# Performance work log

Measured on AMD Instinct MI355X. Metric: run time of the kernel, lower is better.

## Reference

```python
import jax, jax.numpy as jnp
import numpy as np

OPS_SIZE = (40, 40, 40)
ALPHA = 0.005
BETA = 0.01


def _disp_from_landmarks(coords, values):
    # coords, values: (N,3). Returns (3, W0, H0, D0) coarse displacement field.
    D0, H0, W0 = OPS_SIZE
    axes = [jnp.linspace(-1.0, 1.0, s) for s in OPS_SIZE]
    grid = jnp.stack(jnp.meshgrid(*axes, indexing='ij'), -1).reshape(-1, 3)  # (G,3)
    # squared distance ||g - c||^2 via expansion (avoids (N,G,3) repeat tensor)
    d2 = (jnp.sum(grid * grid, -1)[:, None]
          + jnp.sum(coords * coords, -1)[None, :]
          - 2.0 * grid @ coords.T)  # (G,N)
    w = jnp.exp(-d2 / ALPHA)
    w = (BETA + 1.0) * w / (jnp.sum(w, axis=1, keepdims=True) + BETA)
    disp = (w @ values).reshape(D0, H0, W0, 3)
    return jnp.transpose(disp, (3, 2, 1, 0))  # torch permute(3,2,1,0)


def _interp_axis(x, axis, out_s):
    # 1D linear resize along `axis`, matching F.interpolate align_corners=False
    in_s = x.shape[axis]
    c = jnp.maximum((jnp.arange(out_s, dtype=jnp.float32) + 0.5) * (in_s / out_s) - 0.5, 0.0)
    i0 = jnp.minimum(jnp.floor(c).astype(jnp.int32), in_s - 1)
    i1 = jnp.minimum(i0 + 1, in_s - 1)
    t = (c - i0.astype(jnp.float32)).astype(x.dtype)
    shp = [1] * x.ndim
    shp[axis] = out_s
    t = t.reshape(shp)
    return jnp.take(x, i0, axis=axis) * (1 - t) + jnp.take(x, i1, axis=axis) * t


def _resize_trilinear(x, out_size):
    # x: (C, d, h, w) -> (C, D, H, W); trilinear resize is separable
    for ax, s in zip((1, 2, 3), out_size):
        x = _interp_axis(x, ax, s)
    return x


def _grid_sample_3d(vol, grid):
    # vol: (B,C,D,H,W), grid: (B,Do,Ho,Wo,3), grid[...,0]=x indexes W.
    # mode='bilinear' (trilinear), padding_mode='zeros', align_corners=False
    B, C, D, H, W = vol.shape
    x = ((grid[..., 0] + 1.0) * W - 1.0) / 2.0
    y = ((grid[..., 1] + 1.0) * H - 1.0) / 2.0
    z = ((grid[..., 2] + 1.0) * D - 1.0) / 2.0

    def per_batch(v, x, y, z):
        x0 = jnp.floor(x); y0 = jnp.floor(y); z0 = jnp.floor(z)
        fx = x - x0; fy = y - y0; fz = z - z0
        x0i = x0.astype(jnp.int32); y0i = y0.astype(jnp.int32); z0i = z0.astype(jnp.int32)
        acc = jnp.zeros((C,) + x.shape, v.dtype)
        for dz in (0, 1):
            wz = fz if dz else 1.0 - fz
            zi = z0i + dz
            for dy in (0, 1):
                wy = fy if dy else 1.0 - fy
                yi = y0i + dy
                for dx in (0, 1):
                    wx = fx if dx else 1.0 - fx
                    xi = x0i + dx
                    m = ((zi >= 0) & (zi < D) & (yi >= 0) & (yi < H) & (xi >= 0) & (xi < W)).astype(v.dtype)
                    zc = jnp.clip(zi, 0, D - 1); yc = jnp.clip(yi, 0, H - 1); xc = jnp.clip(xi, 0, W - 1)
                    acc = acc + v[:, zc, yc, xc] * ((wz * wy * wx * m)[None])
        return acc

    return jax.vmap(per_batch)(vol, x, y, z)


def reference(orgin_mask, control_points_coords, control_points_offsets):
    B, C, D, H, W = orgin_mask.shape
    coords = control_points_coords + control_points_offsets  # (B,N,3)
    vals = -control_points_offsets                            # (B,N,3)
    disp = jax.vmap(_disp_from_landmarks)(coords, vals)       # (B,3,W0,H0,D0)
    flow = jax.vmap(lambda d: _resize_trilinear(d, (D, H, W)))(disp)  # (B,3,D,H,W)
    axes = [jnp.linspace(-1.0, 1.0, s) for s in (D, H, W)]
    base = jnp.stack(jnp.meshgrid(*axes, indexing='ij'), 0)   # (3,D,H,W)
    base = jnp.transpose(base, (0, 3, 2, 1))                  # torch permute(0,1,4,3,2); needs D==H==W
    warped = base[None] + flow                                # (B,3,D,H,W)
    warped = jnp.transpose(warped, (0, 2, 3, 4, 1))           # (B,D,H,W,3)
    return _grid_sample_3d(orgin_mask, warped)


def setup_inputs() -> dict:
    key = jax.random.key(0)
    k1, k2, k3 = jax.random.split(key, 3)
    orgin_mask = jax.random.uniform(k1, (2, 1, 128, 128, 128), dtype=jnp.float32)
    control_points_coords = jax.random.uniform(k2, (2, 1024, 3), dtype=jnp.float32, minval=-1.0, maxval=1.0)
    control_points_offsets = jax.random.normal(k3, (2, 1024, 3), dtype=jnp.float32) * 0.05
    return {"orgin_mask": orgin_mask,
            "control_points_coords": control_points_coords,
            "control_points_offsets": control_points_offsets}
```

## Files before the change

kernel.cpp:

```cpp
#include <hip/hip_runtime.h>
#include <math.h>
#include <string.h>

#define NLM   1024
#define NB    2
#define OPS   40
#define DIM   128
#define OPS3  (OPS*OPS*OPS)
#define DIM3  (DIM*DIM*DIM)

#define P_T 4
#define Q_T 4
#define R_T 8
#define NP  (OPS/P_T)
#define NQ  (OPS/Q_T)
#define NR  (OPS/R_T)
#define MARGIN 0.30f

#define K2f  (-288.5390081777927f)
#define M2f  ( 577.0780163555854f)


__device__ __forceinline__ float fexp2(float x) {
#if __has_builtin(__builtin_amdgcn_exp2f)
    return __builtin_amdgcn_exp2f(x);
#else
    return exp2f(x);
#endif
}

__global__ __launch_bounds__(128)
void coarse_kernel(const float* __restrict__ coords, const float* __restrict__ offs,
                   float4* __restrict__ C) {
    __shared__ float4 sA[NLM];
    __shared__ float4 sV[NLM];
    __shared__ int sCnt;

    const int t = threadIdx.x;
    const int b = blockIdx.y;
    const int tile = blockIdx.x;
    const int tp = tile / (NQ*NR);
    const int tq = (tile / NR) % NQ;
    const int tr = tile % NR;

    const float step = 2.f / (OPS - 1);
    const float bx0 = -1.f + step * (tr*R_T)          - MARGIN;
    const float bx1 = -1.f + step * (tr*R_T + R_T-1)  + MARGIN;
    const float by0 = -1.f + step * (tq*Q_T)          - MARGIN;
    const float by1 = -1.f + step * (tq*Q_T + Q_T-1)  + MARGIN;
    const float bz0 = -1.f + step * (tp*P_T)          - MARGIN;
    const float bz1 = -1.f + step * (tp*P_T + P_T-1)  + MARGIN;

    if (t == 0) sCnt = 0;
    __syncthreads();

    for (int n = t; n < NLM; n += 128) {
        const float* cp = coords + (b*NLM + n)*3;
        const float* op = offs   + (b*NLM + n)*3;
        float ox = op[0], oy = op[1], oz = op[2];
        float cx = cp[0] + ox, cy = cp[1] + oy, cz = cp[2] + oz;
        if (cx >= bx0 && cx <= bx1 && cy >= by0 && cy <= by1 &&
            cz >= bz0 && cz <= bz1) {
            int idx = atomicAdd(&sCnt, 1);
            sA[idx] = make_float4(cx, cy, cz, K2f*(cx*cx + cy*cy + cz*cz));
            sV[idx] = make_float4(-ox, -oy, -oz, 0.f);
        }
    }
    __syncthreads();
    const int cnt = sCnt;

    const int lp = t >> 5;
    const int lq = (t >> 3) & 3;
    const int lr = t & 7;
    const float gx = -1.f + step * (tr*R_T + lr);
    const float gy = -1.f + step * (tq*Q_T + lq);
    const float gz = -1.f + step * (tp*P_T + lp);
    const float h  = K2f * (gx*gx + gy*gy + gz*gz);

    float aS = 0.f, aX = 0.f, aY = 0.f, aZ = 0.f;
    for (int n = 0; n < cnt; ++n) {
        float4 a = sA[n];
        float4 v = sV[n];
        float u   = fmaf(gx, a.x, fmaf(gy, a.y, gz*a.z));
        float arg = fmaf(M2f, u, h + a.w);
        float e   = fexp2(arg);
        aS += e;
        aX = fmaf(e, v.x, aX);
        aY = fmaf(e, v.y, aY);
        aZ = fmaf(e, v.z, aZ);
    }

    const int p = tp*P_T + lp, q = tq*Q_T + lq, r = tr*R_T + lr;
    const float inv = 1.01f / (aS + 0.01f);
    C[b*OPS3 + (p*OPS + q)*OPS + r] = make_float4(aX*inv, aY*inv, aZ*inv, 0.f);
}

__device__ __forceinline__ void axis_interp(int t, int& a0, int& a1, float& w) {
    float c = fmaxf(0.3125f * (float)t - 0.34375f, 0.f);
    float f = floorf(c);
    a0 = (int)f;
    a1 = min(a0 + 1, OPS - 1);
    w = c - f;
}

__device__ __forceinline__ float4 lerp4(float4 a, float4 b, float t) {
    return make_float4(a.x + t*(b.x - a.x),
                       a.y + t*(b.y - a.y),
                       a.z + t*(b.z - a.z),
                       0.f);
}

typedef float vf2 __attribute__((ext_vector_type(2)));

#if __has_builtin(__builtin_amdgcn_make_buffer_rsrc) && \
    __has_builtin(__builtin_amdgcn_raw_ptr_buffer_load_b64)
#define USE_BUF 1
typedef unsigned int v2u __attribute__((ext_vector_type(2)));
__device__ __forceinline__ vf2 bload2(__amdgpu_buffer_rsrc_t R, int voff_bytes) {
    v2u r = __builtin_amdgcn_raw_ptr_buffer_load_b64(R, voff_bytes, 0, 0);
    vf2 f;
    memcpy(&f, &r, 8);
    return f;
}
#else
#define USE_BUF 0
struct __attribute__((packed, aligned(4))) P2 { vf2 v; };
__device__ __forceinline__ vf2 load2(const float* p) {
    return ((const P2*)p)->v;
}
#endif

struct AW {
    int r0, r1, r2, r3, xs;
    float e0, e1, wy0, wy1, wz0, wz1;
};

__device__ __forceinline__ AW make_aw(float px, float py, float pz) {
    AW s;
    float xf = floorf(px), yf = floorf(py), zf = floorf(pz);
    int x0 = (int)xf, y0 = (int)yf, z0 = (int)zf;
    float ax = px - xf, ay = py - yf, az = pz - zf;

    float wx0 = ((unsigned)x0     < 128u) ? (1.f - ax) : 0.f;
    float wx1 = ((unsigned)(x0+1) < 128u) ? ax         : 0.f;
    s.wy0 = ((unsigned)y0     < 128u) ? (1.f - ay) : 0.f;
    s.wy1 = ((unsigned)(y0+1) < 128u) ? ay         : 0.f;
    s.wz0 = ((unsigned)z0     < 128u) ? (1.f - az) : 0.f;
    s.wz1 = ((unsigned)(z0+1) < 128u) ? az         : 0.f;

    s.xs = min(max(x0, 0), 126);
    int d = x0 - s.xs;
    s.e0 = (d == 0) ? wx0 : ((d == -1) ? wx1 : 0.f);
    s.e1 = (d == 0) ? wx1 : ((d ==  1) ? wx0 : 0.f);

#if USE_BUF
    int ya = y0 << 7, yb2 = (y0+1) << 7;
    int za = z0 << 14, zb2 = (z0+1) << 14;
#else
    int ya = (y0 & 127) << 7, yb2 = ((y0+1) & 127) << 7;
    int za = (z0 & 127) << 14, zb2 = ((z0+1) & 127) << 14;
#endif
    s.r0 = za + ya;  s.r1 = za + yb2;
    s.r2 = zb2 + ya; s.r3 = zb2 + yb2;
    return s;
}

__global__ __launch_bounds__(512)
void warp_kernel(const float* __restrict__ mask, const float4* __restrict__ C,
                 float* __restrict__ out) {
    __shared__ float4 sF[8][OPS];

    const int g = blockIdx.x;
    const int w = threadIdx.x >> 6;
    const int lane = threadIdx.x & 63;
    const int line = ((g & 7) << 12) + ((g >> 3) << 3) + w;
    const int j = line & (DIM-1);
    const int i = (line >> 7) & (DIM-1);
    const int b = line >> 14;

    int i0,i1,j0,j1; float ti,tj;
    axis_interp(i, i0, i1, ti);
    axis_interp(j, j0, j1, tj);

    const float4* Cb = C + b*OPS3;
    if (lane < OPS) {
        float4 c00 = Cb[(i0*OPS + j0)*OPS + lane];
        float4 c01 = Cb[(i0*OPS + j1)*OPS + lane];
        float4 c10 = Cb[(i1*OPS + j0)*OPS + lane];
        float4 c11 = Cb[(i1*OPS + j1)*OPS + lane];
        sF[w][lane] = lerp4(lerp4(c00, c01, tj), lerp4(c10, c11, tj), ti);
    }

    const float* M = mask + b * DIM3;
#if USE_BUF
    __amdgpu_buffer_rsrc_t R =
        __builtin_amdgcn_make_buffer_rsrc((void*)M, (short)0,
                                          DIM3 * 4, 0x00020000);
#endif
    const float s127 = 2.f / (DIM - 1);
    const float yb = -1.f + s127 * (float)j;
    const float zb = -1.f + s127 * (float)i;

    AW aw[2];
    #pragma unroll
    for (int c = 0; c < 2; ++c) {
        const int k = lane + (c << 6);
        int k0,k1; float tk;
        axis_interp(k, k0, k1, tk);
        float4 fl = lerp4(sF[w][k0], sF[w][k1], tk);
        float x = -1.f + s127 * (float)k + fl.x;
        float y = yb + fl.y;
        float z = zb + fl.z;
        aw[c] = make_aw(((x + 1.f) * (float)DIM - 1.f) * 0.5f,
                        ((y + 1.f) * (float)DIM - 1.f) * 0.5f,
                        ((z + 1.f) * (float)DIM - 1.f) * 0.5f);
    }

    vf2 t0[4], t1[4];
#if USE_BUF
    {
        const AW& s = aw[0];
        t0[0] = bload2(R, (s.r0 + s.xs) * 4);
        t0[1] = bload2(R, (s.r1 + s.xs) * 4);
        t0[2] = bload2(R, (s.r2 + s.xs) * 4);
        t0[3] = bload2(R, (s.r3 + s.xs) * 4);
    }
    {
        const AW& s = aw[1];
        t1[0] = bload2(R, (s.r0 + s.xs) * 4);
        t1[1] = bload2(R, (s.r1 + s.xs) * 4);
        t1[2] = bload2(R, (s.r2 + s.xs) * 4);
        t1[3] = bload2(R, (s.r3 + s.xs) * 4);
    }
#else
    {
        const AW& s = aw[0];
        t0[0] = load2(M + s.r0 + s.xs);
        t0[1] = load2(M + s.r1 + s.xs);
        t0[2] = load2(M + s.r2 + s.xs);
        t0[3] = load2(M + s.r3 + s.xs);
    }
    {
        const AW& s = aw[1];
        t1[0] = load2(M + s.r0 + s.xs);
        t1[1] = load2(M + s.r1 + s.xs);
        t1[2] = load2(M + s.r2 + s.xs);
        t1[3] = load2(M + s.r3 + s.xs);
    }
#endif

    float res[2];
    #pragma unroll
    for (int c = 0; c < 2; ++c) {
        const AW& s = aw[c];
        const vf2* tv = c ? t1 : t0;
        vf2 e;  e.x = s.e0;  e.y = s.e1;
        vf2 acc;
        acc    = tv[0] * (e * (s.wz0*s.wy0));
        acc   += tv[1] * (e * (s.wz0*s.wy1));
        acc   += tv[2] * (e * (s.wz1*s.wy0));
        acc   += tv[3] * (e * (s.wz1*s.wy1));
        res[c] = acc.x + acc.y;
    }
    out[(line << 7) + lane]      = res[0];
    out[(line << 7) + lane + 64] = res[1];
}

extern "C" void kernel_launch(void* const* d_in, const int* in_sizes, int n_in,
                              void* d_out, int out_size, void* d_ws, size_t ws_size,
                              hipStream_t stream) {
    const float* mask   = (const float*)d_in[0];
    const float* coords = (const float*)d_in[1];
    const float* offs   = (const float*)d_in[2];
    float* out = (float*)d_out;

    float4* coarse = (float4*)d_ws;

    dim3 g1(NP*NQ*NR, NB);
    coarse_kernel<<<g1, 128, 0, stream>>>(coords, offs, coarse);

    warp_kernel<<<NB*DIM*DIM/8, 512, 0, stream>>>(mask, coarse, out);
}
```

Before: 98.35 us.

## Assign adjacent x pairs per thread and share one 16-byte gather

Each thread now handles two adjacent output voxels along x instead of two voxels 64 apart. When both samples fall in the same y/z cell and adjacent x columns, four 128-bit loads replace eight 64-bit loads, and the outputs are written as one float2 store. Otherwise it falls back to the old eight-load path. Block size also drops from 512 to 256 threads with a matching grid, which adds a divergent branch and changes the occupancy mix.

```diff
diff --git a/kernel.cpp b/kernel.cpp
--- a/kernel.cpp
+++ b/kernel.cpp
@@ -111,27 +111,33 @@
 }
 
 typedef float vf2 __attribute__((ext_vector_type(2)));
+typedef float vf4 __attribute__((ext_vector_type(4)));
 
 #if __has_builtin(__builtin_amdgcn_make_buffer_rsrc) && \
-    __has_builtin(__builtin_amdgcn_raw_ptr_buffer_load_b64)
+    __has_builtin(__builtin_amdgcn_raw_ptr_buffer_load_b64) && \
+    __has_builtin(__builtin_amdgcn_raw_ptr_buffer_load_b128)
 #define USE_BUF 1
 typedef unsigned int v2u __attribute__((ext_vector_type(2)));
+typedef unsigned int v4u __attribute__((ext_vector_type(4)));
 __device__ __forceinline__ vf2 bload2(__amdgpu_buffer_rsrc_t R, int voff_bytes) {
     v2u r = __builtin_amdgcn_raw_ptr_buffer_load_b64(R, voff_bytes, 0, 0);
-    vf2 f;
-    memcpy(&f, &r, 8);
-    return f;
+    vf2 f; memcpy(&f, &r, 8); return f;
+}
+__device__ __forceinline__ vf4 bload4(__amdgpu_buffer_rsrc_t R, int voff_bytes) {
+    v4u r = __builtin_amdgcn_raw_ptr_buffer_load_b128(R, voff_bytes, 0, 0);
+    vf4 f; memcpy(&f, &r, 16); return f;
 }
 #else
 #define USE_BUF 0
 struct __attribute__((packed, aligned(4))) P2 { vf2 v; };
-__device__ __forceinline__ vf2 load2(const float* p) {
-    return ((const P2*)p)->v;
-}
+struct __attribute__((packed, aligned(4))) P4 { vf4 v; };
+__device__ __forceinline__ vf2 load2(const float* p) { return ((const P2*)p)->v; }
+__device__ __forceinline__ vf4 load4(const float* p) { return ((const P4*)p)->v; }
 #endif
 
 struct AW {
     int r0, r1, r2, r3, xs;
+    int y0, z0;
     float e0, e1, wy0, wy1, wz0, wz1;
 };
 
@@ -153,6 +159,7 @@
     s.e0 = (d == 0) ? wx0 : ((d == -1) ? wx1 : 0.f);
     s.e1 = (d == 0) ? wx1 : ((d ==  1) ? wx0 : 0.f);
 
+    s.y0 = y0; s.z0 = z0;
 #if USE_BUF
     int ya = y0 << 7, yb2 = (y0+1) << 7;
     int za = z0 << 14, zb2 = (z0+1) << 14;
@@ -165,15 +172,15 @@
     return s;
 }
 
-__global__ __launch_bounds__(512)
+__global__ __launch_bounds__(256)
 void warp_kernel(const float* __restrict__ mask, const float4* __restrict__ C,
                  float* __restrict__ out) {
-    __shared__ float4 sF[8][OPS];
+    __shared__ float4 sF[4][OPS];
 
     const int g = blockIdx.x;
     const int w = threadIdx.x >> 6;
     const int lane = threadIdx.x & 63;
-    const int line = ((g & 7) << 12) + ((g >> 3) << 3) + w;
+    const int line = ((g & 7) << 12) + ((g >> 3) << 2) + w;
     const int j = line & (DIM-1);
     const int i = (line >> 7) & (DIM-1);
     const int b = line >> 14;
@@ -204,7 +211,7 @@
     AW aw[2];
     #pragma unroll
     for (int c = 0; c < 2; ++c) {
-        const int k = lane + (c << 6);
+        const int k = (lane << 1) + c;
         int k0,k1; float tk;
         axis_interp(k, k0, k1, tk);
         float4 fl = lerp4(sF[w][k0], sF[w][k1], tk);
@@ -216,54 +223,92 @@
                         ((z + 1.f) * (float)DIM - 1.f) * 0.5f);
     }
 
-    vf2 t0[4], t1[4];
+    const AW& A = aw[0];
+    const AW& B = aw[1];
+    const bool fast = (A.y0 == B.y0) & (A.z0 == B.z0) &
+                      (B.xs - A.xs == 1) & (A.xs <= 124);
+
+    float resA, resB;
+    if (fast) {
+        vf4 T0, T1, T2, T3;
 #if USE_BUF
-    {
-        const AW& s = aw[0];
-        t0[0] = bload2(R, (s.r0 + s.xs) * 4);
-        t0[1] = bload2(R, (s.r1 + s.xs) * 4);
-        t0[2] = bload2(R, (s.r2 + s.xs) * 4);
-        t0[3] = bload2(R, (s.r3 + s.xs) * 4);
-    }
-    {
-        const AW& s = aw[1];
-        t1[0] = bload2(R, (s.r0 + s.xs) * 4);
-        t1[1] = bload2(R, (s.r1 + s.xs) * 4);
-        t1[2] = bload2(R, (s.r2 + s.xs) * 4);
-        t1[3] = bload2(R, (s.r3 + s.xs) * 4);
-    }
-#else
-    {
-        const AW& s = aw[0];
-        t0[0] = load2(M + s.r0 + s.xs);
-        t0[1] = load2(M + s.r1 + s.xs);
-        t0[2] = load2(M + s.r2 + s.xs);
-        t0[3] = load2(M + s.r3 + s.xs);
-    }
-    {
-        const AW& s = aw[1];
-        t1[0] = load2(M + s.r0 + s.xs);
-        t1[1] = load2(M + s.r1 + s.xs);
-        t1[2] = load2(M + s.r2 + s.xs);
-        t1[3] = load2(M + s.r3 + s.xs);
-    }
-#endif
-
-    float res[2];
-    #pragma unroll
-    for (int c = 0; c < 2; ++c) {
-        const AW& s = aw[c];
-        const vf2* tv = c ? t1 : t0;
-        vf2 e;  e.x = s.e0;  e.y = s.e1;
-        vf2 acc;
-        acc    = tv[0] * (e * (s.wz0*s.wy0));
-        acc   += tv[1] * (e * (s.wz0*s.wy1));
-        acc   += tv[2] * (e * (s.wz1*s.wy0));
-        acc   += tv[3] * (e * (s.wz1*s.wy1));
-        res[c] = acc.x + acc.y;
-    }
-    out[(line << 7) + lane]      = res[0];
-    out[(line << 7) + lane + 64] = res[1];
+        T0 = bload4(R, (A.r0 + A.xs) * 4);
+        T1 = bload4(R, (A.r1 + A.xs) * 4);
+        T2 = bload4(R, (A.r2 + A.xs) * 4);
+        T3 = bload4(R, (A.r3 + A.xs) * 4);
+#else
+        T0 = load4(M + A.r0 + A.xs);
+        T1 = load4(M + A.r1 + A.xs);
+        T2 = load4(M + A.r2 + A.xs);
+        T3 = load4(M + A.r3 + A.xs);
+#endif
+        float a0 = A.wz0*A.wy0, a1 = A.wz0*A.wy1;
+        float a2 = A.wz1*A.wy0, a3 = A.wz1*A.wy1;
+        float b0 = B.wz0*B.wy0, b1 = B.wz0*B.wy1;
+        float b2 = B.wz1*B.wy0, b3 = B.wz1*B.wy1;
+        float rA;
+        rA = T0.x * (a0*A.e0);
+        rA = fmaf(T0.y, a0*A.e1, rA);
+        rA = fmaf(T1.x, a1*A.e0, rA);
+        rA = fmaf(T1.y, a1*A.e1, rA);
+        rA = fmaf(T2.x, a2*A.e0, rA);
+        rA = fmaf(T2.y, a2*A.e1, rA);
+        rA = fmaf(T3.x, a3*A.e0, rA);
+        rA = fmaf(T3.y, a3*A.e1, rA);
+        float rB;
+        rB = T0.y * (b0*B.e0);
+        rB = fmaf(T0.z, b0*B.e1, rB);
+        rB = fmaf(T1.y, b1*B.e0, rB);
+        rB = fmaf(T1.z, b1*B.e1, rB);
+        rB = fmaf(T2.y, b2*B.e0, rB);
+        rB = fmaf(T2.z, b2*B.e1, rB);
+        rB = fmaf(T3.y, b3*B.e0, rB);
+        rB = fmaf(T3.z, b3*B.e1, rB);
+        resA = rA; resB = rB;
+    } else {
+        vf2 t0[4], t1[4];
+#if USE_BUF
+        t0[0] = bload2(R, (A.r0 + A.xs) * 4);
+        t0[1] = bload2(R, (A.r1 + A.xs) * 4);
+        t0[2] = bload2(R, (A.r2 + A.xs) * 4);
+        t0[3] = bload2(R, (A.r3 + A.xs) * 4);
+        t1[0] = bload2(R, (B.r0 + B.xs) * 4);
+        t1[1] = bload2(R, (B.r1 + B.xs) * 4);
+        t1[2] = bload2(R, (B.r2 + B.xs) * 4);
+        t1[3] = bload2(R, (B.r3 + B.xs) * 4);
+#else
+        t0[0] = load2(M + A.r0 + A.xs);
+        t0[1] = load2(M + A.r1 + A.xs);
+        t0[2] = load2(M + A.r2 + A.xs);
+        t0[3] = load2(M + A.r3 + A.xs);
+        t1[0] = load2(M + B.r0 + B.xs);
+        t1[1] = load2(M + B.r1 + B.xs);
+        t1[2] = load2(M + B.r2 + B.xs);
+        t1[3] = load2(M + B.r3 + B.xs);
+#endif
+        float rA;
+        rA = t0[0].x * (A.wz0*A.wy0*A.e0);
+        rA = fmaf(t0[0].y, A.wz0*A.wy0*A.e1, rA);
+        rA = fmaf(t0[1].x, A.wz0*A.wy1*A.e0, rA);
+        rA = fmaf(t0[1].y, A.wz0*A.wy1*A.e1, rA);
+        rA = fmaf(t0[2].x, A.wz1*A.wy0*A.e0, rA);
+        rA = fmaf(t0[2].y, A.wz1*A.wy0*A.e1, rA);
+        rA = fmaf(t0[3].x, A.wz1*A.wy1*A.e0, rA);
+        rA = fmaf(t0[3].y, A.wz1*A.wy1*A.e1, rA);
+        float rB;
+        rB = t1[0].x * (B.wz0*B.wy0*B.e0);
+        rB = fmaf(t1[0].y, B.wz0*B.wy0*B.e1, rB);
+        rB = fmaf(t1[1].x, B.wz0*B.wy1*B.e0, rB);
+        rB = fmaf(t1[1].y, B.wz0*B.wy1*B.e1, rB);
+        rB = fmaf(t1[2].x, B.wz1*B.wy0*B.e0, rB);
+        rB = fmaf(t1[2].y, B.wz1*B.wy0*B.e1, rB);
+        rB = fmaf(t1[3].x, B.wz1*B.wy1*B.e0, rB);
+        rB = fmaf(t1[3].y, B.wz1*B.wy1*B.e1, rB);
+        resA = rA; resB = rB;
+    }
+
+    vf2 o; o.x = resA; o.y = resB;
+    *(vf2*)(out + (line << 7) + (lane << 1)) = o;
 }
 
 extern "C" void kernel_launch(void* const* d_in, const int* in_sizes, int n_in,
@@ -279,5 +324,5 @@
     dim3 g1(NP*NQ*NR, NB);
     coarse_kernel<<<g1, 128, 0, stream>>>(coords, offs, coarse);
 
-    warp_kernel<<<NB*DIM*DIM/8, 512, 0, stream>>>(mask, coarse, out);
-}
+    warp_kernel<<<NB*DIM*DIM/4, 256, 0, stream>>>(mask, coarse, out);
+}
```

After: 102.2 us. 4.0% more time.
